# Optimization experiments

Hardware: AMD Instinct MI355X
Metric: run time of the kernel (lower is better)

Reference implementation:

```python
import jax, jax.numpy as jnp
import numpy as np

K = 49        # k_neighbors
EPS = 1e-5    # BatchNorm2d eps


def setup_inputs() -> dict:
    key = jax.random.key(0)
    ks = jax.random.split(key, 2)
    B, C, M, O = 64, 64, 32, 128
    X = jax.random.normal(ks[0], (B, C, M, M), dtype=jnp.float32)
    # conv1x1 weight (kaiming fan_out) flattened to (O, C); bias init 0
    W = jax.random.normal(ks[1], (O, C), dtype=jnp.float32) * (2.0 / O) ** 0.5
    b = jnp.zeros((O,), jnp.float32)
    gamma = jnp.ones((O,), jnp.float32)
    beta = jnp.zeros((O,), jnp.float32)
    run_mean = jnp.zeros((O,), jnp.float32)
    run_var = jnp.ones((O,), jnp.float32)
    return dict(X=X, W=W, b=b, gamma=gamma, beta=beta,
                run_mean=run_mean, run_var=run_var)


def _knn_aggregate(x):
    """x: (N, C) node features -> D^{-1/2} A D^{-1/2} x for the kNN graph."""
    N = x.shape[0]
    sq = jnp.sum(x * x, axis=1)
    d2 = sq[:, None] + sq[None, :] - 2.0 * (x @ x.T)
    dist = jnp.sqrt(jnp.maximum(d2, 0.0))              # torch.cdist (p=2)
    i = jnp.arange(N)
    dist = dist.at[i, i].set(jnp.inf)                  # fill_diagonal_(inf)
    _, knn = jax.lax.top_k(-dist, K)                   # (N, K) nearest indices
    # topk indices are distinct -> every row degree == K, and the column
    # normalizer uses the col node's row degree (also K), so
    # D^{-1/2} A D^{-1/2} x == mean of gathered neighbors.
    nb = x[knn]                                        # (N, K, C) gather
    return nb.sum(axis=1) / K


def reference(X, W, b, gamma, beta, run_mean, run_var):
    B, C, M, _ = X.shape
    N = M * M
    x = X.reshape(B, C, N).transpose(0, 2, 1)          # (B, N, C) nodes
    Z = jax.vmap(_knn_aggregate)(x)                    # (B, N, C) sparse GCN agg
    # 1x1 conv over the (M, M) grid == per-node linear map
    Fg = jnp.einsum('oc,bnc->bon', W, Z) + b[None, :, None]   # (B, O, N)
    Fg = jax.nn.relu(Fg)
    # BatchNorm2d with running stats (eval mode); Dropout2d is identity in eval
    inv = jax.lax.rsqrt(run_var + EPS)
    Fg = gamma[None, :, None] * (Fg - run_mean[None, :, None]) * inv[None, :, None] + beta[None, :, None]
    return Fg.mean(axis=2)                             # AdaptiveAvgPool2d(1) -> (B, O)
```

## Files before the change

kernel.cpp:

```cpp
#include <hip/hip_runtime.h>
#include <stdint.h>

#define BATCH 64
#define CDIM  64
#define NPTS  1024
#define ODIM  128
#define KNN   49
#define KNNP  52
#define BNEPS 1e-5f

typedef __attribute__((ext_vector_type(8))) short bf16x8;
typedef __attribute__((ext_vector_type(4))) float f32x4;

#define O_XF   0
#define SZ_XF  (BATCH*64*2*64*8*4)
#define O_SQ   (O_XF + SZ_XF)
#define SZ_SQ  (BATCH*NPTS*4)
#define O_KNN  (O_SQ + SZ_SQ)
#define SZ_KNN (BATCH*NPTS*KNNP*4)
#define O_Z    (O_KNN + SZ_KNN)
#define SZ_Z   (BATCH*NPTS*CDIM*4)
#define WS_NEED ((size_t)(O_Z + SZ_Z))

__global__ void gcn_init(const float* __restrict__ gamma, const float* __restrict__ beta,
                         const float* __restrict__ rmean, const float* __restrict__ rvar,
                         float* __restrict__ out) {
    int i = blockIdx.x * 256 + threadIdx.x;
    if (i < BATCH * ODIM) {
        int o = i & (ODIM - 1);
        out[i] = beta[o] - gamma[o] * rmean[o] * rsqrtf(rvar[o] + BNEPS);
    }
}

__global__ __launch_bounds__(256) void k0_split(const float* __restrict__ X,
                                                uint32_t* __restrict__ XF,
                                                float* __restrict__ sq) {
    const int b    = blockIdx.x >> 4;
    const int t16  = (blockIdx.x & 15) * 4 + (threadIdx.x >> 6);
    const int lane = threadIdx.x & 63;
    const int n    = t16 * 16 + (lane & 15);
    const int cg   = lane >> 4;
    const float* Xb = X + (size_t)b * CDIM * NPTS;
    float s = 0.f;
    for (int ks = 0; ks < 2; ks++) {
        uint32_t hi[4], lo[4];
#pragma unroll
        for (int dj = 0; dj < 4; dj++) {
            uint32_t hw[2], lw[2];
#pragma unroll
            for (int e = 0; e < 2; e++) {
                int c = ks * 32 + cg * 8 + dj * 2 + e;
                float x = Xb[(size_t)c * NPTS + n];
                s += x * x;
                uint32_t u  = __float_as_uint(x);
                uint32_t hr = (u + 0x7FFFu + ((u >> 16) & 1u)) >> 16;
                float    hf = __uint_as_float(hr << 16);
                uint32_t ul = __float_as_uint(x - hf);
                uint32_t lr = (ul + 0x7FFFu + ((ul >> 16) & 1u)) >> 16;
                hw[e] = hr; lw[e] = lr;
            }
            hi[dj] = hw[0] | (hw[1] << 16);
            lo[dj] = lw[0] | (lw[1] << 16);
        }
        size_t entry = ((size_t)(b * 64 + t16) * 2 + ks) * 64 + lane;
        uint32_t* p = XF + entry * 8;
        *(uint4*)p       = make_uint4(hi[0], hi[1], hi[2], hi[3]);
        *(uint4*)(p + 4) = make_uint4(lo[0], lo[1], lo[2], lo[3]);
    }
    s += __shfl_xor(s, 16, 64);
    s += __shfl_xor(s, 32, 64);
    if (lane < 16) sq[b * NPTS + n] = s;
}

__global__ __launch_bounds__(512, 6) void k1_gram_select(const uint32_t* __restrict__ XF,
                                                         const float* __restrict__ sq,
                                                         int* __restrict__ knn) {
    __shared__ uint32_t s_pk[8 * 1024];
    const int b    = blockIdx.x >> 6;
    const int rt   = blockIdx.x & 63;
    const int wave = threadIdx.x >> 6, lane = threadIdx.x & 63;
    const int q = lane >> 4, l15 = lane & 15;

    bf16x8 ahi[2], alo[2];
#pragma unroll
    for (int ks = 0; ks < 2; ks++) {
        const uint32_t* p = XF + (((size_t)(b * 64 + rt) * 2 + ks) * 64 + lane) * 8;
        ahi[ks] = *(const bf16x8*)p;
        alo[ks] = *(const bf16x8*)(p + 4);
    }
    const float* sqb = sq + b * NPTS;

#pragma unroll
    for (int tt = 0; tt < 8; tt++) {
        const int t16 = wave * 8 + tt;
        f32x4 acc = {0.f, 0.f, 0.f, 0.f};
#pragma unroll
        for (int ks = 0; ks < 2; ks++) {
            const uint32_t* p = XF + (((size_t)(b * 64 + t16) * 2 + ks) * 64 + lane) * 8;
            bf16x8 bhi = *(const bf16x8*)p;
            bf16x8 blo = *(const bf16x8*)(p + 4);
            acc = __builtin_amdgcn_mfma_f32_16x16x32_bf16(ahi[ks], bhi, acc, 0, 0, 0);
            acc = __builtin_amdgcn_mfma_f32_16x16x32_bf16(alo[ks], bhi, acc, 0, 0, 0);
            acc = __builtin_amdgcn_mfma_f32_16x16x32_bf16(ahi[ks], blo, acc, 0, 0, 0);
        }
        const int col  = t16 * 16 + l15;
        const float sqv = sqb[col];
        uint32_t k16[4];
#pragma unroll
        for (int i = 0; i < 4; i++) {
            int row = q * 4 + i;
            float d = sqv - 2.f * acc[i];
            if (col == rt * 16 + row) d = __uint_as_float(0x7F800000u);
            uint32_t u = __float_as_uint(d);
            uint32_t key = ((int)u < 0) ? ~u : (u | 0x80000000u);
            k16[i] = key >> 16;
        }
        const int p0 = 2 * q, p1 = 2 * q + 1;
        s_pk[p0 * 1024 + (col ^ ((p0 & 3) << 3))] = k16[0] | (k16[1] << 16);
        s_pk[p1 * 1024 + (col ^ ((p1 & 3) << 3))] = k16[2] | (k16[3] << 16);
    }
    __syncthreads();

    uint32_t k0r[16], k1r[16];
    {
        const int sw = (wave & 3) << 3;
#pragma unroll
        for (int tt = 0; tt < 16; tt++) {
            uint32_t pk = s_pk[wave * 1024 + ((tt * 64 + lane) ^ sw)];
            k0r[tt] = pk & 0xFFFFu;
            k1r[tt] = pk >> 16;
        }
    }

    uint32_t lo0, hi0, lo1, hi1;
    {
        uint32_t lm0 = k0r[0], lm1 = k1r[0];
#pragma unroll
        for (int tt = 1; tt < 16; tt++) {
            lm0 = k0r[tt] < lm0 ? k0r[tt] : lm0;
            lm1 = k1r[tt] < lm1 ? k1r[tt] : lm1;
        }
        uint32_t g0 = lm0, m0 = lm0, g1 = lm1, m1 = lm1;
#pragma unroll
        for (int off = 1; off < 64; off <<= 1) {
            uint32_t a0 = (uint32_t)__shfl_xor((int)g0, off, 64);
            uint32_t b0 = (uint32_t)__shfl_xor((int)m0, off, 64);
            uint32_t a1 = (uint32_t)__shfl_xor((int)g1, off, 64);
            uint32_t b1 = (uint32_t)__shfl_xor((int)m1, off, 64);
            g0 = a0 < g0 ? a0 : g0;  m0 = b0 > m0 ? b0 : m0;
            g1 = a1 < g1 ? a1 : g1;  m1 = b1 > m1 ? b1 : m1;
        }
        lo0 = g0; hi0 = m0;
        lo1 = g1; hi1 = m1;
    }

    for (int it = 0; it < 16; it++) {
        bool a0 = lo0 < hi0, a1 = lo1 < hi1;
        if (!a0 && !a1) break;
        uint32_t mid0 = (lo0 + hi0) >> 1;
        uint32_t mid1 = (lo1 + hi1) >> 1;
        int cnt0 = 0, cnt1 = 0;
#pragma unroll
        for (int tt = 0; tt < 16; tt++) {
            cnt0 += __popcll(__ballot(k0r[tt] <= mid0));
            cnt1 += __popcll(__ballot(k1r[tt] <= mid1));
        }
        if (a0) { if (cnt0 >= KNN) hi0 = mid0; else lo0 = mid0 + 1; }
        if (a1) { if (cnt1 >= KNN) hi1 = mid1; else lo1 = mid1 + 1; }
    }

    const unsigned long long ltmask = (1ull << lane) - 1ull;
#pragma unroll
    for (int r = 0; r < 2; r++) {
        const int row = wave * 2 + r;
        const uint32_t vstar = r ? lo1 : lo0;
        const uint32_t* k = r ? k1r : k0r;
        int cntless = 0;
#pragma unroll
        for (int tt = 0; tt < 16; tt++)
            cntless += __popcll(__ballot(k[tt] < vstar));
        const int need = KNN - cntless;
        int base = 0, eqtaken = 0;
        int* kout = knn + ((size_t)b * NPTS + rt * 16 + row) * KNNP;
#pragma unroll
        for (int tt = 0; tt < 16; tt++) {
            bool islt = k[tt] < vstar, iseq = k[tt] == vstar;
            unsigned long long meq = __ballot(iseq);
            int eqrank = eqtaken + __popcll(meq & ltmask);
            bool sel = islt || (iseq && eqrank < need);
            unsigned long long msel = __ballot(sel);
            if (sel) kout[base + __popcll(msel & ltmask)] = tt * 64 + lane;
            base    += __popcll(msel);
            eqtaken += __popcll(meq);
        }
    }
}

__global__ __launch_bounds__(256) void k2a_aggregate(const float* __restrict__ X,
                                                     const int* __restrict__ knn,
                                                     float* __restrict__ z) {
    __shared__ float XT[16 * 1024];
    const int b = blockIdx.x >> 3, cg = (blockIdx.x >> 1) & 3, half = blockIdx.x & 1;
    const int t = threadIdx.x;
    const float* Xb = X + ((size_t)b * CDIM + cg * 16) * NPTS;
#pragma unroll
    for (int nn = 0; nn < 4; nn++) {
        int n = nn * 256 + t;
#pragma unroll
        for (int g = 0; g < 4; g++) {
            float4 v;
            v.x = Xb[(size_t)(4 * g + 0) * NPTS + n];
            v.y = Xb[(size_t)(4 * g + 1) * NPTS + n];
            v.z = Xb[(size_t)(4 * g + 2) * NPTS + n];
            v.w = Xb[(size_t)(4 * g + 3) * NPTS + n];
            int qp = g ^ ((n >> 1) & 3);
            *(float4*)&XT[n * 16 + qp * 4] = v;
        }
    }
    __syncthreads();
    const int wave = t >> 6, lane = t & 63;
    const int r2 = lane >> 4, kb = (lane >> 2) & 3, g = lane & 3;
    for (int rr = 0; rr < 32; rr++) {
        const int row = half * 512 + wave * 128 + rr * 4 + r2;
        const int* kr = knn + ((size_t)b * NPTS + row) * KNNP;
        float4 s = {0.f, 0.f, 0.f, 0.f};
#pragma unroll
        for (int cs = 0; cs < 3; cs++) {
            int4 j4 = *(const int4*)&kr[(kb + 4 * cs) * 4];
            int js[4] = {j4.x, j4.y, j4.z, j4.w};
#pragma unroll
            for (int e = 0; e < 4; e++) {
                int j = js[e];
                float4 v = *(const float4*)&XT[j * 16 + ((g ^ ((j >> 1) & 3)) << 2)];
                s.x += v.x; s.y += v.y; s.z += v.z; s.w += v.w;
            }
        }
        if (kb == 0) {
            int j = kr[48];
            float4 v = *(const float4*)&XT[j * 16 + ((g ^ ((j >> 1) & 3)) << 2)];
            s.x += v.x; s.y += v.y; s.z += v.z; s.w += v.w;
        }
#pragma unroll
        for (int off = 4; off <= 8; off <<= 1) {
            s.x += __shfl_xor(s.x, off, 64);
            s.y += __shfl_xor(s.y, off, 64);
            s.z += __shfl_xor(s.z, off, 64);
            s.w += __shfl_xor(s.w, off, 64);
        }
        if (kb == 0)
            *(float4*)&z[((size_t)b * NPTS + row) * CDIM + cg * 16 + g * 4] = s;
    }
}

__global__ __launch_bounds__(256) void k2b_gemm(const float* __restrict__ z,
                                                const float* __restrict__ W,
                                                const float* __restrict__ bias,
                                                const float* __restrict__ gamma,
                                                const float* __restrict__ rvar,
                                                float* __restrict__ out) {
    __shared__ __align__(16) float s_zz[128 * 64];
    __shared__ float s_red[2][256];
    const int b = blockIdx.x >> 3, nq = blockIdx.x & 7;
    const int t = threadIdx.x;
    const float* zb = z + ((size_t)b * NPTS + nq * 128) * CDIM;
#pragma unroll
    for (int qq = 0; qq < 8; qq++) {
        int e = qq * 256 + t;
        *(float4*)&s_zz[e * 4] = *(const float4*)&zb[e * 4];
    }
    __syncthreads();
    const int o2 = t & 63, h = t >> 6;
    float4 w0[16], w1[16];
#pragma unroll
    for (int c4 = 0; c4 < 16; c4++) {
        w0[c4] = *(const float4*)&W[(size_t)o2 * CDIM + c4 * 4];
        w1[c4] = *(const float4*)&W[(size_t)(o2 + 64) * CDIM + c4 * 4];
    }
    const float b0 = bias[o2], b1 = bias[o2 + 64];
    float r0 = 0.f, r1 = 0.f;
    for (int r = 0; r < 32; r++) {
        const float* zr = &s_zz[(h * 32 + r) * 64];
        float a0 = 0.f, a1 = 0.f;
#pragma unroll
        for (int c4 = 0; c4 < 16; c4++) {
            float4 zv = *(const float4*)&zr[c4 * 4];
            a0 += w0[c4].x * zv.x + w0[c4].y * zv.y + w0[c4].z * zv.z + w0[c4].w * zv.w;
            a1 += w1[c4].x * zv.x + w1[c4].y * zv.y + w1[c4].z * zv.z + w1[c4].w * zv.w;
        }
        r0 += fmaxf(a0 * (1.f / KNN) + b0, 0.f);
        r1 += fmaxf(a1 * (1.f / KNN) + b1, 0.f);
    }
    s_red[0][t] = r0; s_red[1][t] = r1;
    __syncthreads();
    if (t < 128) {
        const int oo = t & 63, which = t >> 6;
        const int o = which * 64 + oo;
        float sum = s_red[which][oo] + s_red[which][64 + oo] +
                    s_red[which][128 + oo] + s_red[which][192 + oo];
        float scale = gamma[o] * rsqrtf(rvar[o] + BNEPS) * (1.f / NPTS);
        atomicAdd(&out[b * ODIM + o], sum * scale);
    }
}

#define RTILE 8
#define APAD  1028
#define WPAD  132
#define POOLF (64 * WPAD)

__global__ __launch_bounds__(256) void gcn_main(
    const float* __restrict__ X, const float* __restrict__ W,
    const float* __restrict__ bias, const float* __restrict__ gamma,
    const float* __restrict__ rvar, float* __restrict__ out)
{
    __shared__ __align__(16) float s_pool[POOLF];
    __shared__ __align__(16) float s_fstage[4][APAD];
    __shared__ int   s_knn[RTILE][KNN];
    __shared__ float s_z[RTILE][CDIM];

    const int t = threadIdx.x;
    const int b = blockIdx.x >> 7;
    const int rtile = blockIdx.x & 127;
    const int r0 = rtile * RTILE;
    const float* Xb = X + (size_t)b * CDIM * NPTS;

    float acc[RTILE][4];
    float sqv[4];
#pragma unroll
    for (int r = 0; r < RTILE; r++)
#pragma unroll
        for (int u = 0; u < 4; u++) acc[r][u] = 0.f;
#pragma unroll
    for (int u = 0; u < 4; u++) sqv[u] = 0.f;

    for (int ch = 0; ch < 16; ch++) {
        const int c0 = ch * 4;
#pragma unroll
        for (int cc = 0; cc < 4; cc++) {
            float4 v = *(const float4*)(Xb + (size_t)(c0 + cc) * NPTS + 4 * t);
            *(float4*)&s_fstage[cc][4 * t] = v;
        }
        __syncthreads();
#pragma unroll
        for (int cc = 0; cc < 4; cc++) {
            float4 bv4 = *(const float4*)&s_fstage[cc][4 * t];
            float bv[4] = {bv4.x, bv4.y, bv4.z, bv4.w};
#pragma unroll
            for (int u = 0; u < 4; u++) sqv[u] += bv[u] * bv[u];
            const float* arow = Xb + (size_t)(c0 + cc) * NPTS + r0;
            float4 a0 = *(const float4*)(arow);
            float4 a1 = *(const float4*)(arow + 4);
            float av[8] = {a0.x, a0.y, a0.z, a0.w, a1.x, a1.y, a1.z, a1.w};
#pragma unroll
            for (int r = 0; r < RTILE; r++)
#pragma unroll
                for (int u = 0; u < 4; u++) acc[r][u] += av[r] * bv[u];
        }
        __syncthreads();
    }

    float* s_dist = s_pool;
#pragma unroll
    for (int r = 0; r < RTILE; r++) {
        const int rG = r0 + r;
        float d[4];
#pragma unroll
        for (int u = 0; u < 4; u++) {
            float dd = sqv[u] - 2.f * acc[r][u];
            d[u] = (4 * t + u == rG) ? __uint_as_float(0x7F800000u) : dd;
        }
        *(float4*)&s_dist[r * NPTS + 4 * t] = make_float4(d[0], d[1], d[2], d[3]);
    }
    __syncthreads();

    const int wave = t >> 6, lane = t & 63;
    const unsigned long long ltmask = (1ull << lane) - 1ull;
    for (int rr = 0; rr < 2; rr++) {
        const int row = wave * 2 + rr;
        unsigned key[16];
#pragma unroll
        for (int tt = 0; tt < 16; tt++) {
            unsigned u = __float_as_uint(s_dist[row * NPTS + tt * 64 + lane]);
            key[tt] = (u & 0x80000000u) ? ~u : (u | 0x80000000u);
        }
        unsigned lo = 0u, hi = 0xFFFFFFFFu;
        while (lo < hi) {
            unsigned mid = lo + ((hi - lo) >> 1);
            int cnt = 0;
#pragma unroll
            for (int tt = 0; tt < 16; tt++)
                cnt += __popcll(__ballot(key[tt] <= mid));
            if (cnt >= KNN) hi = mid; else lo = mid + 1;
        }
        const unsigned v49 = lo;
        int cntless = 0;
#pragma unroll
        for (int tt = 0; tt < 16; tt++)
            cntless += __popcll(__ballot(key[tt] < v49));
        const int need = KNN - cntless;
        int base = 0, eqtaken = 0;
#pragma unroll
        for (int tt = 0; tt < 16; tt++) {
            bool islt = key[tt] < v49;
            bool iseq = key[tt] == v49;
            unsigned long long meq = __ballot(iseq);
            int eqrank = eqtaken + __popcll(meq & ltmask);
            bool sel = islt || (iseq && (eqrank < need));
            unsigned long long msel = __ballot(sel);
            if (sel) {
                int pos = base + __popcll(msel & ltmask);
                s_knn[row][pos] = tt * 64 + lane;
            }
            base    += __popcll(msel);
            eqtaken += __popcll(meq);
        }
    }
    __syncthreads();

    float* astage = s_pool;
    float* s_redf = (float*)s_fstage;
    const int ar = t >> 5, acc8 = (t & 31) >> 2, ks = t & 3;
    for (int c0 = 0; c0 < CDIM; c0 += 8) {
#pragma unroll
        for (int qq = 0; qq < 8; qq++) {
            int if4 = qq * 256 + t;
            int cc = if4 >> 8, j4 = if4 & 255;
            float4 v = *(const float4*)(Xb + (size_t)(c0 + cc) * NPTS + 4 * j4);
            *(float4*)&astage[cc * APAD + 4 * j4] = v;
        }
        __syncthreads();
        float partial = 0.f;
        for (int k = ks; k < KNN; k += 4)
            partial += astage[acc8 * APAD + s_knn[ar][k]];
        s_redf[t] = partial;
        __syncthreads();
        if (t < 64) {
            int r = t >> 3, cc = t & 7;
            int bi = r * 32 + cc * 4;
            s_z[r][c0 + cc] = s_redf[bi] + s_redf[bi + 1] + s_redf[bi + 2] + s_redf[bi + 3];
        }
        __syncthreads();
    }

    float* wt = s_pool;
#pragma unroll 4
    for (int qq = 0; qq < 32; qq++) {
        int e = qq * 256 + t;
        int o = e >> 6, c = e & 63;
        wt[c * WPAD + o] = W[e];
    }
    __syncthreads();
    const int o = t & 127, rg = t >> 7;
    float facc[4] = {0.f, 0.f, 0.f, 0.f};
    for (int c = 0; c < CDIM; c += 4) {
        float w0 = wt[(c + 0) * WPAD + o], w1 = wt[(c + 1) * WPAD + o];
        float w2 = wt[(c + 2) * WPAD + o], w3 = wt[(c + 3) * WPAD + o];
#pragma unroll
        for (int qq = 0; qq < 4; qq++) {
            float4 zv = *(const float4*)&s_z[rg * 4 + qq][c];
            facc[qq] += w0 * zv.x + w1 * zv.y + w2 * zv.z + w3 * zv.w;
        }
    }
    const float bo = bias[o];
    float rsum = 0.f;
#pragma unroll
    for (int qq = 0; qq < 4; qq++) {
        float f = facc[qq] * (1.f / KNN) + bo;
        rsum += fmaxf(f, 0.f);
    }
    s_redf[t] = rsum;
    __syncthreads();
    if (t < 128) {
        float scale = gamma[t] * rsqrtf(rvar[t] + BNEPS) * (1.f / NPTS);
        atomicAdd(&out[b * ODIM + t], (s_redf[t] + s_redf[t + 128]) * scale);
    }
}

extern "C" void kernel_launch(void* const* d_in, const int* in_sizes, int n_in,
                              void* d_out, int out_size, void* d_ws, size_t ws_size,
                              hipStream_t stream) {
    const float* X     = (const float*)d_in[0];
    const float* W     = (const float*)d_in[1];
    const float* bias  = (const float*)d_in[2];
    const float* gamma = (const float*)d_in[3];
    const float* beta  = (const float*)d_in[4];
    const float* rmean = (const float*)d_in[5];
    const float* rvar  = (const float*)d_in[6];
    float* out = (float*)d_out;

    gcn_init<<<(BATCH * ODIM + 255) / 256, 256, 0, stream>>>(gamma, beta, rmean, rvar, out);
    if (ws_size >= WS_NEED) {
        uint8_t* ws = (uint8_t*)d_ws;
        uint32_t* XF  = (uint32_t*)(ws + O_XF);
        float*    sqw = (float*)(ws + O_SQ);
        int*      knn = (int*)(ws + O_KNN);
        float*    zw  = (float*)(ws + O_Z);
        k0_split<<<BATCH * 16, 256, 0, stream>>>(X, XF, sqw);
        k1_gram_select<<<BATCH * 64, 512, 0, stream>>>(XF, sqw, knn);
        k2a_aggregate<<<BATCH * 8, 256, 0, stream>>>(X, knn, zw);
        k2b_gemm<<<BATCH * 8, 256, 0, stream>>>(zw, W, bias, gamma, rvar, out);
    } else {
        gcn_main<<<BATCH * (NPTS / RTILE), 256, 0, stream>>>(X, W, bias, gamma, rvar, out);
    }
}
```

Before: 285.5 us.

## Halve k1 block size with four rows per wave and prefix-scan kNN emission

k1_gram_select now runs 256-thread blocks in which each wave computes 16 Gram tiles and then selects the top-k for four rows instead of two. This batches the radix-bisection ballots across more rows. The ballot-per-element emission loop is replaced by per-lane local counts plus a single packed shuffle prefix scan, and key packing uses perm and xor tricks. k2a_aggregate merges its two halves into one 512-thread block, so the X tile is staged into shared memory once per (batch, channel group) rather than twice. The costs are higher register pressure from the 4x16 key array, fewer k2a blocks to fill the GPU, and a different tie ordering within the kNN output.

```diff
diff --git a/kernel.cpp b/kernel.cpp
--- a/kernel.cpp
+++ b/kernel.cpp
@@ -72,7 +72,7 @@
     if (lane < 16) sq[b * NPTS + n] = s;
 }
 
-__global__ __launch_bounds__(512, 6) void k1_gram_select(const uint32_t* __restrict__ XF,
+__global__ __launch_bounds__(256, 4) void k1_gram_select(const uint32_t* __restrict__ XF,
                                                          const float* __restrict__ sq,
                                                          int* __restrict__ knn) {
     __shared__ uint32_t s_pk[8 * 1024];
@@ -89,10 +89,11 @@
         alo[ks] = *(const bf16x8*)(p + 4);
     }
     const float* sqb = sq + b * NPTS;
-
-#pragma unroll
-    for (int tt = 0; tt < 8; tt++) {
-        const int t16 = wave * 8 + tt;
+    const int swq = (q & 1) << 4;
+
+#pragma unroll
+    for (int tt = 0; tt < 16; tt++) {
+        const int t16 = wave * 16 + tt;
         f32x4 acc = {0.f, 0.f, 0.f, 0.f};
 #pragma unroll
         for (int ks = 0; ks < 2; ks++) {
@@ -105,107 +106,128 @@
         }
         const int col  = t16 * 16 + l15;
         const float sqv = sqb[col];
-        uint32_t k16[4];
+        float d[4];
+#pragma unroll
+        for (int i = 0; i < 4; i++)
+            d[i] = fmaf(-2.f, acc[i], sqv);
+        if (t16 == rt) {
+#pragma unroll
+            for (int i = 0; i < 4; i++)
+                if (l15 == q * 4 + i) d[i] = __uint_as_float(0x7F800000u);
+        }
+        uint32_t key[4];
 #pragma unroll
         for (int i = 0; i < 4; i++) {
-            int row = q * 4 + i;
-            float d = sqv - 2.f * acc[i];
-            if (col == rt * 16 + row) d = __uint_as_float(0x7F800000u);
-            uint32_t u = __float_as_uint(d);
-            uint32_t key = ((int)u < 0) ? ~u : (u | 0x80000000u);
-            k16[i] = key >> 16;
-        }
-        const int p0 = 2 * q, p1 = 2 * q + 1;
-        s_pk[p0 * 1024 + (col ^ ((p0 & 3) << 3))] = k16[0] | (k16[1] << 16);
-        s_pk[p1 * 1024 + (col ^ ((p1 & 3) << 3))] = k16[2] | (k16[3] << 16);
-    }
-    __syncthreads();
-
-    uint32_t k0r[16], k1r[16];
+            uint32_t u = __float_as_uint(d[i]);
+            key[i] = u ^ (uint32_t)(((int)u >> 31) | 0x80000000);
+        }
+        uint32_t pk01 = __builtin_amdgcn_perm(key[1], key[0], 0x07060302);
+        uint32_t pk23 = __builtin_amdgcn_perm(key[3], key[2], 0x07060302);
+        s_pk[(2 * q) * 1024 + (col ^ swq)]     = pk01;
+        s_pk[(2 * q + 1) * 1024 + (col ^ swq)] = pk23;
+    }
+    __syncthreads();
+
+    uint32_t k[4][16];
     {
-        const int sw = (wave & 3) << 3;
+        const int swr = (wave & 1) << 4;
 #pragma unroll
         for (int tt = 0; tt < 16; tt++) {
-            uint32_t pk = s_pk[wave * 1024 + ((tt * 64 + lane) ^ sw)];
-            k0r[tt] = pk & 0xFFFFu;
-            k1r[tt] = pk >> 16;
-        }
-    }
-
-    uint32_t lo0, hi0, lo1, hi1;
+            uint32_t a  = s_pk[(2 * wave) * 1024 + ((tt * 64 + lane) ^ swr)];
+            uint32_t bb = s_pk[(2 * wave + 1) * 1024 + ((tt * 64 + lane) ^ swr)];
+            k[0][tt] = a & 0xFFFFu;  k[1][tt] = a >> 16;
+            k[2][tt] = bb & 0xFFFFu; k[3][tt] = bb >> 16;
+        }
+    }
+
+    uint32_t lo[4], hi[4];
     {
-        uint32_t lm0 = k0r[0], lm1 = k1r[0];
-#pragma unroll
-        for (int tt = 1; tt < 16; tt++) {
-            lm0 = k0r[tt] < lm0 ? k0r[tt] : lm0;
-            lm1 = k1r[tt] < lm1 ? k1r[tt] : lm1;
-        }
-        uint32_t g0 = lm0, m0 = lm0, g1 = lm1, m1 = lm1;
+        uint32_t lmin[4];
+#pragma unroll
+        for (int r = 0; r < 4; r++) {
+            uint32_t m = k[r][0];
+#pragma unroll
+            for (int tt = 1; tt < 16; tt++) m = k[r][tt] < m ? k[r][tt] : m;
+            lmin[r] = m;
+        }
+#pragma unroll
+        for (int r = 0; r < 4; r++) { lo[r] = lmin[r]; hi[r] = lmin[r]; }
 #pragma unroll
         for (int off = 1; off < 64; off <<= 1) {
-            uint32_t a0 = (uint32_t)__shfl_xor((int)g0, off, 64);
-            uint32_t b0 = (uint32_t)__shfl_xor((int)m0, off, 64);
-            uint32_t a1 = (uint32_t)__shfl_xor((int)g1, off, 64);
-            uint32_t b1 = (uint32_t)__shfl_xor((int)m1, off, 64);
-            g0 = a0 < g0 ? a0 : g0;  m0 = b0 > m0 ? b0 : m0;
-            g1 = a1 < g1 ? a1 : g1;  m1 = b1 > m1 ? b1 : m1;
-        }
-        lo0 = g0; hi0 = m0;
-        lo1 = g1; hi1 = m1;
+#pragma unroll
+            for (int r = 0; r < 4; r++) {
+                uint32_t a = (uint32_t)__shfl_xor((int)lo[r], off, 64);
+                uint32_t m = (uint32_t)__shfl_xor((int)hi[r], off, 64);
+                lo[r] = a < lo[r] ? a : lo[r];
+                hi[r] = m > hi[r] ? m : hi[r];
+            }
+        }
     }
 
     for (int it = 0; it < 16; it++) {
-        bool a0 = lo0 < hi0, a1 = lo1 < hi1;
-        if (!a0 && !a1) break;
-        uint32_t mid0 = (lo0 + hi0) >> 1;
-        uint32_t mid1 = (lo1 + hi1) >> 1;
-        int cnt0 = 0, cnt1 = 0;
+        bool act0 = lo[0] < hi[0], act1 = lo[1] < hi[1];
+        bool act2 = lo[2] < hi[2], act3 = lo[3] < hi[3];
+        if (!act0 && !act1 && !act2 && !act3) break;
+        uint32_t mid[4];
+        int cnt[4] = {0, 0, 0, 0};
+#pragma unroll
+        for (int r = 0; r < 4; r++) mid[r] = (lo[r] + hi[r]) >> 1;
 #pragma unroll
         for (int tt = 0; tt < 16; tt++) {
-            cnt0 += __popcll(__ballot(k0r[tt] <= mid0));
-            cnt1 += __popcll(__ballot(k1r[tt] <= mid1));
-        }
-        if (a0) { if (cnt0 >= KNN) hi0 = mid0; else lo0 = mid0 + 1; }
-        if (a1) { if (cnt1 >= KNN) hi1 = mid1; else lo1 = mid1 + 1; }
-    }
-
-    const unsigned long long ltmask = (1ull << lane) - 1ull;
-#pragma unroll
-    for (int r = 0; r < 2; r++) {
-        const int row = wave * 2 + r;
-        const uint32_t vstar = r ? lo1 : lo0;
-        const uint32_t* k = r ? k1r : k0r;
-        int cntless = 0;
-#pragma unroll
-        for (int tt = 0; tt < 16; tt++)
-            cntless += __popcll(__ballot(k[tt] < vstar));
-        const int need = KNN - cntless;
-        int base = 0, eqtaken = 0;
-        int* kout = knn + ((size_t)b * NPTS + rt * 16 + row) * KNNP;
+            cnt[0] += __popcll(__ballot(k[0][tt] <= mid[0]));
+            cnt[1] += __popcll(__ballot(k[1][tt] <= mid[1]));
+            cnt[2] += __popcll(__ballot(k[2][tt] <= mid[2]));
+            cnt[3] += __popcll(__ballot(k[3][tt] <= mid[3]));
+        }
+#pragma unroll
+        for (int r = 0; r < 4; r++)
+            if (lo[r] < hi[r]) {
+                if (cnt[r] >= KNN) hi[r] = mid[r]; else lo[r] = mid[r] + 1;
+            }
+    }
+
+#pragma unroll
+    for (int r = 0; r < 4; r++) {
+        const uint32_t vstar = lo[r];
+        int loc_lt = 0, loc_eq = 0;
 #pragma unroll
         for (int tt = 0; tt < 16; tt++) {
-            bool islt = k[tt] < vstar, iseq = k[tt] == vstar;
-            unsigned long long meq = __ballot(iseq);
-            int eqrank = eqtaken + __popcll(meq & ltmask);
-            bool sel = islt || (iseq && eqrank < need);
-            unsigned long long msel = __ballot(sel);
-            if (sel) kout[base + __popcll(msel & ltmask)] = tt * 64 + lane;
-            base    += __popcll(msel);
-            eqtaken += __popcll(meq);
-        }
-    }
-}
-
-__global__ __launch_bounds__(256) void k2a_aggregate(const float* __restrict__ X,
+            loc_lt += (k[r][tt] < vstar);
+            loc_eq += (k[r][tt] == vstar);
+        }
+        uint32_t v = (uint32_t)loc_lt | ((uint32_t)loc_eq << 16);
+#pragma unroll
+        for (int off = 1; off < 64; off <<= 1) {
+            uint32_t u = (uint32_t)__shfl_up((int)v, off, 64);
+            if (lane >= off) v += u;
+        }
+        uint32_t tot = (uint32_t)__shfl((int)v, 63, 64);
+        const int total_lt = (int)(tot & 0xFFFFu);
+        int p_lt = (int)(v & 0xFFFFu) - loc_lt;
+        int p_eq = total_lt + ((int)(v >> 16) - loc_eq);
+        int* kout = knn + ((size_t)b * NPTS + rt * 16 + 4 * wave + r) * KNNP;
+#pragma unroll
+        for (int tt = 0; tt < 16; tt++) {
+            bool islt = k[r][tt] < vstar;
+            bool iseq = k[r][tt] == vstar;
+            int pos = islt ? p_lt : p_eq;
+            bool wv = islt || (iseq && p_eq < KNN);
+            if (wv) kout[pos] = tt * 64 + lane;
+            p_lt += islt; p_eq += iseq;
+        }
+    }
+}
+
+__global__ __launch_bounds__(512) void k2a_aggregate(const float* __restrict__ X,
                                                      const int* __restrict__ knn,
                                                      float* __restrict__ z) {
     __shared__ float XT[16 * 1024];
-    const int b = blockIdx.x >> 3, cg = (blockIdx.x >> 1) & 3, half = blockIdx.x & 1;
+    const int b = blockIdx.x >> 2, cg = blockIdx.x & 3;
     const int t = threadIdx.x;
     const float* Xb = X + ((size_t)b * CDIM + cg * 16) * NPTS;
 #pragma unroll
-    for (int nn = 0; nn < 4; nn++) {
-        int n = nn * 256 + t;
+    for (int nn = 0; nn < 2; nn++) {
+        int n = nn * 512 + t;
 #pragma unroll
         for (int g = 0; g < 4; g++) {
             float4 v;
@@ -221,7 +243,7 @@
     const int wave = t >> 6, lane = t & 63;
     const int r2 = lane >> 4, kb = (lane >> 2) & 3, g = lane & 3;
     for (int rr = 0; rr < 32; rr++) {
-        const int row = half * 512 + wave * 128 + rr * 4 + r2;
+        const int row = wave * 128 + rr * 4 + r2;
         const int* kr = knn + ((size_t)b * NPTS + row) * KNNP;
         float4 s = {0.f, 0.f, 0.f, 0.f};
 #pragma unroll
@@ -495,8 +517,8 @@
         int*      knn = (int*)(ws + O_KNN);
         float*    zw  = (float*)(ws + O_Z);
         k0_split<<<BATCH * 16, 256, 0, stream>>>(X, XF, sqw);
-        k1_gram_select<<<BATCH * 64, 512, 0, stream>>>(XF, sqw, knn);
-        k2a_aggregate<<<BATCH * 8, 256, 0, stream>>>(X, knn, zw);
+        k1_gram_select<<<BATCH * 64, 256, 0, stream>>>(XF, sqw, knn);
+        k2a_aggregate<<<BATCH * 4, 512, 0, stream>>>(X, knn, zw);
         k2b_gemm<<<BATCH * 8, 256, 0, stream>>>(zw, W, bias, gamma, rvar, out);
     } else {
         gcn_main<<<BATCH * (NPTS / RTILE), 256, 0, stream>>>(X, W, bias, gamma, rvar, out);
```

After: 285.7 us. Within noise of the previous version (+0.1%).
